# Performance work log

Measured on AMD Instinct MI355X. Metric: run time of the kernel, lower is better.

Reference implementation:

```python
import jax, jax.numpy as jnp
import numpy as np

N_NODES = 100000


def _sage_conv(x, edge_index, W_l, b_l, W_r):
    # PyG SAGEConv (aggr='mean', root_weight=True, normalize=False):
    # out = lin_l(mean_{j in N(i)} x_j) + lin_r(x_i)
    src, dst = edge_index[0], edge_index[1]
    n = x.shape[0]
    agg = jax.ops.segment_sum(x[src], dst, num_segments=n)
    cnt = jax.ops.segment_sum(jnp.ones((src.shape[0],), x.dtype), dst, num_segments=n)
    agg = agg / jnp.maximum(cnt, 1.0)[:, None]
    return agg @ W_l + b_l + x @ W_r


def setup_inputs() -> dict:
    key = jax.random.key(0)
    ks = jax.random.split(key, 12)
    in_dim, hidden = 384, 128
    x = jax.random.normal(ks[0], (N_NODES, in_dim), dtype=jnp.float32)
    edge_index = jax.random.randint(ks[1], (2, 3200000), 0, N_NODES, dtype=jnp.int32)
    pos_edge_label_index = jax.random.randint(ks[2], (2, 500000), 0, N_NODES, dtype=jnp.int32)
    neg_edge_label_index = jax.random.randint(ks[3], (2, 500000), 0, N_NODES, dtype=jnp.int32)
    s1 = 1.0 / np.sqrt(in_dim)
    s2 = 1.0 / np.sqrt(hidden)
    return {
        "x": x,
        "edge_index": edge_index,
        "pos_edge_label_index": pos_edge_label_index,
        "neg_edge_label_index": neg_edge_label_index,
        "W_l1": jax.random.uniform(ks[4], (in_dim, hidden), jnp.float32, -s1, s1),
        "b_l1": jnp.zeros((hidden,), jnp.float32),
        "W_r1": jax.random.uniform(ks[5], (in_dim, hidden), jnp.float32, -s1, s1),
        "W_l2": jax.random.uniform(ks[6], (hidden, hidden), jnp.float32, -s2, s2),
        "b_l2": jnp.zeros((hidden,), jnp.float32),
        "W_r2": jax.random.uniform(ks[7], (hidden, hidden), jnp.float32, -s2, s2),
        "W_lin": jax.random.uniform(ks[8], (2 * hidden, 1), jnp.float32, -s2, s2),
        "b_lin": jnp.zeros((1,), jnp.float32),
    }


def reference(x, edge_index, pos_edge_label_index, neg_edge_label_index,
              W_l1, b_l1, W_r1, W_l2, b_l2, W_r2, W_lin, b_lin):
    h = _sage_conv(x, edge_index, W_l1, b_l1, W_r1)
    h = jax.nn.relu(h)
    h = _sage_conv(h, edge_index, W_l2, b_l2, W_r2)

    def score(idx):
        pair = jnp.concatenate([h[idx[0]], h[idx[1]]], axis=1)  # [E, 2*hidden]
        return (pair @ W_lin + b_lin).reshape(-1)

    return score(pos_edge_label_index), score(neg_edge_label_index)
```

## Files before the change

kernel.cpp:

```cpp
#include <hip/hip_runtime.h>

#define IN_DIM 384
#define HID    128
#define NPB    256
#define BCAP   16384
#define LCAP   10240

#define AS1 __attribute__((address_space(1)))
#define AS3 __attribute__((address_space(3)))

typedef _Float16 half8 __attribute__((ext_vector_type(8)));
typedef _Float16 half2t __attribute__((ext_vector_type(2)));
typedef __fp16 fp16x2 __attribute__((ext_vector_type(2)));
typedef float floatx4 __attribute__((ext_vector_type(4)));
typedef float floatx2 __attribute__((ext_vector_type(2)));

__global__ void zero_i32(int* __restrict__ p, int n) {
  int i = blockIdx.x * 256 + threadIdx.x;
  if (i < n) p[i] = 0;
}

__global__ __launch_bounds__(512) void partition_kernel(
    const int* __restrict__ src, const int* __restrict__ dst, int E, int nB,
    int* __restrict__ bCur, unsigned* __restrict__ bucketData) {
  __shared__ int hist[391];
  __shared__ int gbase[391];
  const int t = threadIdx.x;
  const int b0 = blockIdx.x * 8192;

  for (int i = t; i < nB; i += 512) hist[i] = 0;
  __syncthreads();
#pragma unroll
  for (int i = 0; i < 16; ++i) {
    int e = b0 + i * 512 + t;
    if (e < E) atomicAdd(&hist[dst[e] >> 8], 1);
  }
  __syncthreads();
  for (int i = t; i < nB; i += 512) {
    int h = hist[i];
    gbase[i] = h ? (i * BCAP + atomicAdd(&bCur[i], h)) : 0;
    hist[i] = 0;
  }
  __syncthreads();
#pragma unroll
  for (int i = 0; i < 16; ++i) {
    int e = b0 + i * 512 + t;
    if (e < E) {
      int d = dst[e];
      int b = d >> 8;
      int r = atomicAdd(&hist[b], 1);
      bucketData[gbase[b] + r] = ((unsigned)(d & 255) << 17) | (unsigned)src[e];
    }
  }
}

__global__ __launch_bounds__(1024) void node_sort3(
    const unsigned* __restrict__ bucketData, const int* __restrict__ bCur,
    int N, int* __restrict__ sorted_src, int* __restrict__ rs, int* __restrict__ re) {
  extern __shared__ unsigned sdata[];
  __shared__ int hist[NPB];
  __shared__ int s[NPB];
  __shared__ int cur[NPB];
  const int b = blockIdx.x;
  const int t = threadIdx.x;
  const int start = b * BCAP;
  const int fill = bCur[b];
  if (t < NPB) hist[t] = 0;
  __syncthreads();
  for (int i = t; i < fill; i += 1024) {
    unsigned d = bucketData[start + i];
    if (i < LCAP) sdata[i] = d;
    atomicAdd(&hist[d >> 17], 1);
  }
  __syncthreads();
  int v = 0;
  if (t < NPB) { v = hist[t]; s[t] = v; }
  __syncthreads();
  for (int off = 1; off < NPB; off <<= 1) {
    int y = (t < NPB && t >= off) ? s[t - off] : 0;
    __syncthreads();
    if (t < NPB) s[t] += y;
    __syncthreads();
  }
  if (t < NPB) {
    int excl = s[t] - v;
    const int node = b * NPB + t;
    if (node < N) {
      rs[node] = start + excl;
      re[node] = start + excl + v;
    }
    cur[t] = start + excl;
  }
  __syncthreads();
  for (int i = t; i < fill; i += 1024) {
    unsigned d = (i < LCAP) ? sdata[i] : bucketData[start + i];
    int p = atomicAdd(&cur[d >> 17], 1);
    sorted_src[p] = (int)(d & 0x1FFFF);
  }
}

__global__ void pack_w2(const float* __restrict__ Wl, const float* __restrict__ Wr,
                        _Float16* __restrict__ Bp) {
  const float* __restrict__ W = blockIdx.z ? Wr : Wl;
  const int tn = blockIdx.x;
  const int ks = blockIdx.y;
  const int KS = gridDim.y;
  const int lane = threadIdx.x;
  const int n = tn * 16 + (lane & 15);
  const int kb = ks * 32 + (lane >> 4) * 8;
  half8 v;
#pragma unroll
  for (int j = 0; j < 8; ++j) v[j] = (_Float16)W[(size_t)(kb + j) * HID + n];
  *(half8*)(Bp + (((size_t)(blockIdx.z * 8 + tn) * KS + ks) * 64 + lane) * 8) = v;
}

__global__ __launch_bounds__(128) void pack_uv(
    const float* __restrict__ Wl2, const float* __restrict__ Wr2,
    const float* __restrict__ bl2, const float* __restrict__ Wlin,
    float* __restrict__ uv) {
  const int i = threadIdx.x;
  float ua = 0.f, ub = 0.f, va = 0.f, vb = 0.f;
  for (int o = 0; o < 128; ++o) {
    float wa = Wlin[o], wb = Wlin[128 + o];
    float l = Wl2[i * 128 + o], r = Wr2[i * 128 + o];
    ua += l * wa; ub += l * wb;
    va += r * wa; vb += r * wb;
  }
  uv[i] = ua; uv[128 + i] = ub; uv[256 + i] = va; uv[384 + i] = vb;
  if (i == 0) {
    float ca = 0.f, cb = 0.f;
    for (int o = 0; o < 128; ++o) {
      ca += bl2[o] * Wlin[o];
      cb += bl2[o] * Wlin[128 + o];
    }
    uv[512] = ca; uv[513] = cb;
  }
}

__device__ inline half2t cvt_pk(float a, float b) {
  fp16x2 r = __builtin_amdgcn_cvt_pkrtz(a, b);
  union { fp16x2 f; half2t h; } c;
  c.f = r;
  return c.h;
}

__global__ __launch_bounds__(512) void gemm_f32a(
    const float* __restrict__ A, int M,
    const _Float16* __restrict__ Bp,
    unsigned char* __restrict__ y8, _Float16* __restrict__ z1) {
  __shared__ float As[128 * 32];

  const int K = IN_DIM, KS = IN_DIM / 32;
  const int tid = threadIdx.x;
  const int lane = tid & 63;
  const int wid = tid >> 6;
  const int quad = lane >> 4;
  const int lm = lane & 15;
  const int row0 = (wid & 1) * 64;
  const int ct0 = (wid >> 1) * 4;
  const int blockRow = blockIdx.x * 128;

  const int srow = lane >> 3;
  const int scol = ((lane & 7) ^ (srow & 7)) * 4;
  const int grow0 = min(blockRow + wid * 16 + srow, M - 1);
  const int grow1 = min(blockRow + wid * 16 + 8 + srow, M - 1);

  floatx4 acc[16];
#pragma unroll
  for (int i = 0; i < 16; ++i) {
    acc[i][0] = 0.f; acc[i][1] = 0.f; acc[i][2] = 0.f; acc[i][3] = 0.f;
  }

  for (int ks = 0; ks < KS; ++ks) {
    const int k0 = ks * 32;
    __syncthreads();
    __builtin_amdgcn_global_load_lds(
        (const AS1 void*)(A + (size_t)grow0 * K + k0 + scol),
        (AS3 void*)(As + (wid * 16) * 32), 16, 0, 0);
    __builtin_amdgcn_global_load_lds(
        (const AS1 void*)(A + (size_t)grow1 * K + k0 + scol),
        (AS3 void*)(As + (wid * 16 + 8) * 32), 16, 0, 0);

    half8 bf[4];
#pragma unroll
    for (int ct = 0; ct < 4; ++ct)
      bf[ct] = *(const half8*)(Bp + (((size_t)(ct0 + ct) * KS + ks) * 64 + lane) * 8);

    __syncthreads();

    half8 af[4];
#pragma unroll
    for (int rt = 0; rt < 4; ++rt) {
      const int row = row0 + rt * 16 + lm;
      const int sw = row & 7;
      const floatx4 fA = *(const floatx4*)&As[(row * 8 + ((quad * 2) ^ sw)) * 4];
      const floatx4 fB = *(const floatx4*)&As[(row * 8 + ((quad * 2 + 1) ^ sw)) * 4];
      half2t h01 = cvt_pk(fA[0], fA[1]);
      half2t h23 = cvt_pk(fA[2], fA[3]);
      half2t h45 = cvt_pk(fB[0], fB[1]);
      half2t h67 = cvt_pk(fB[2], fB[3]);
      half8 a;
      a[0] = h01[0]; a[1] = h01[1]; a[2] = h23[0]; a[3] = h23[1];
      a[4] = h45[0]; a[5] = h45[1]; a[6] = h67[0]; a[7] = h67[1];
      af[rt] = a;
    }
#pragma unroll
    for (int rt = 0; rt < 4; ++rt)
#pragma unroll
      for (int ct = 0; ct < 4; ++ct)
        acc[rt * 4 + ct] =
            __builtin_amdgcn_mfma_f32_16x16x32_f16(af[rt], bf[ct], acc[rt * 4 + ct], 0, 0, 0);
  }

#pragma unroll
  for (int rt = 0; rt < 4; ++rt) {
#pragma unroll
    for (int r = 0; r < 4; ++r) {
      const int gm = blockRow + row0 + rt * 16 + quad * 4 + r;
      if (gm < M) {
#pragma unroll
        for (int ct = 0; ct < 4; ++ct) {
          const int tn = ct0 + ct;
          const float v = acc[rt * 4 + ct][r];
          if (tn < 8) {
            int p = __builtin_amdgcn_cvt_pk_fp8_f32(v, v, 0, false);
            y8[(size_t)gm * 128 + tn * 16 + lm] = (unsigned char)(p & 0xFF);
          } else {
            z1[(size_t)gm * 128 + (tn - 8) * 16 + lm] = (_Float16)v;
          }
        }
      }
    }
  }
}

__device__ inline float2 upk(unsigned u) {
  union { unsigned v; _Float16 h[2]; } c; c.v = u;
  return make_float2((float)c.h[0], (float)c.h[1]);
}

struct f32acc8 { floatx2 a, b, c, d; };
__device__ inline void f8acc(f32acc8& A, uint2 v) {
  A.a += __builtin_amdgcn_cvt_pk_f32_fp8(v.x, false);
  A.b += __builtin_amdgcn_cvt_pk_f32_fp8(v.x, true);
  A.c += __builtin_amdgcn_cvt_pk_f32_fp8(v.y, false);
  A.d += __builtin_amdgcn_cvt_pk_f32_fp8(v.y, true);
}
__device__ inline void f8merge(f32acc8& A, const f32acc8& B) {
  A.a += B.a; A.b += B.b; A.c += B.c; A.d += B.d;
}

__device__ inline f32acc8 gather_rows8(const unsigned char* __restrict__ y8,
                                       const int* __restrict__ sorted_src,
                                       int start, int end, int cl, int slot) {
  f32acc8 A0; A0.a = 0.f; A0.b = 0.f; A0.c = 0.f; A0.d = 0.f;
  f32acc8 A1 = A0;
  int k = start + slot;
  for (; k + 12 < end; k += 16) {
    int s0 = sorted_src[k];
    int s1 = sorted_src[k + 4];
    int s2 = sorted_src[k + 8];
    int s3 = sorted_src[k + 12];
    uint2 v0 = *(const uint2*)(y8 + (size_t)s0 * 128 + cl * 8);
    uint2 v1 = *(const uint2*)(y8 + (size_t)s1 * 128 + cl * 8);
    uint2 v2 = *(const uint2*)(y8 + (size_t)s2 * 128 + cl * 8);
    uint2 v3 = *(const uint2*)(y8 + (size_t)s3 * 128 + cl * 8);
    f8acc(A0, v0);
    f8acc(A1, v1);
    f8acc(A0, v2);
    f8acc(A1, v3);
  }
  if (k + 4 < end) {
    int s0 = sorted_src[k];
    int s1 = sorted_src[k + 4];
    uint2 v0 = *(const uint2*)(y8 + (size_t)s0 * 128 + cl * 8);
    uint2 v1 = *(const uint2*)(y8 + (size_t)s1 * 128 + cl * 8);
    f8acc(A0, v0);
    f8acc(A1, v1);
    k += 8;
  }
  if (k < end) {
    uint2 v = *(const uint2*)(y8 + (size_t)sorted_src[k] * 128 + cl * 8);
    f8acc(A0, v);
  }
  f8merge(A0, A1);
#pragma unroll
  for (int off = 16; off < 64; off <<= 1) {
    f32acc8 o;
    o.a[0] = __shfl_xor(A0.a[0], off, 64); o.a[1] = __shfl_xor(A0.a[1], off, 64);
    o.b[0] = __shfl_xor(A0.b[0], off, 64); o.b[1] = __shfl_xor(A0.b[1], off, 64);
    o.c[0] = __shfl_xor(A0.c[0], off, 64); o.c[1] = __shfl_xor(A0.c[1], off, 64);
    o.d[0] = __shfl_xor(A0.d[0], off, 64); o.d[1] = __shfl_xor(A0.d[1], off, 64);
    f8merge(A0, o);
  }
  return A0;
}

__global__ __launch_bounds__(256) void agg_relu8_dot(
    const unsigned char* __restrict__ y8, const unsigned* __restrict__ z1u,
    const int* __restrict__ sorted_src,
    const int* __restrict__ rs, const int* __restrict__ re,
    const float* __restrict__ bias, const float* __restrict__ uv,
    float2* __restrict__ t, float2* __restrict__ r, int N) {
  const int w = threadIdx.x >> 6;
  const int lane = threadIdx.x & 63;
  const int cl = lane & 15;
  const int slot = lane >> 4;
  const int node = blockIdx.x * 4 + w;
  if (node >= N) return;
  const int start = rs[node];
  const int end = re[node];
  f32acc8 A = gather_rows8(y8, sorted_src, start, end, cl, slot);
  if (slot == 0) {
    const int deg = end - start;
    const float inv = 1.f / (float)max(deg, 1);
    uint4 z4 = *(const uint4*)(z1u + (size_t)node * 64 + cl * 4);
    const unsigned zv[4] = {z4.x, z4.y, z4.z, z4.w};
    const floatx2 av[4] = {A.a, A.b, A.c, A.d};
    float hv[8];
#pragma unroll
    for (int q = 0; q < 4; ++q) {
      const int c = cl * 8 + q * 2;
      float2 z = upk(zv[q]);
      hv[2 * q]     = fmaxf(av[q][0] * inv + bias[c] + z.x, 0.f);
      hv[2 * q + 1] = fmaxf(av[q][1] * inv + bias[c + 1] + z.y, 0.f);
    }
    float ta = 0.f, tb = 0.f, ra = 0.f, rb = 0.f;
#pragma unroll
    for (int j = 0; j < 8; ++j) {
      const int c = cl * 8 + j;
      ta += hv[j] * uv[c];
      tb += hv[j] * uv[128 + c];
      ra += hv[j] * uv[256 + c];
      rb += hv[j] * uv[384 + c];
    }
#pragma unroll
    for (int off = 1; off < 16; off <<= 1) {
      ta += __shfl_xor(ta, off, 64);
      tb += __shfl_xor(tb, off, 64);
      ra += __shfl_xor(ra, off, 64);
      rb += __shfl_xor(rb, off, 64);
    }
    if (cl == 0) {
      t[node] = make_float2(ta, tb);
      r[node] = make_float2(ra + uv[512], rb + uv[513]);
    }
  }
}

__global__ __launch_bounds__(256) void agg_t(
    const float2* __restrict__ t, const int* __restrict__ sorted_src,
    const int* __restrict__ rs, const int* __restrict__ re,
    const float2* __restrict__ r,
    float* __restrict__ sa, float* __restrict__ sb, int N) {
  const int w = threadIdx.x >> 6;
  const int lane = threadIdx.x & 63;
  const int es = lane & 15;
  const int ns = lane >> 4;
  const int node = blockIdx.x * 16 + w * 4 + ns;
  if (node >= N) return;
  const int start = rs[node];
  const int end = re[node];
  float a = 0.f, b = 0.f;
  for (int k = start + es; k < end; k += 16) {
    float2 v = t[sorted_src[k]];
    a += v.x;
    b += v.y;
  }
#pragma unroll
  for (int off = 1; off < 16; off <<= 1) {
    a += __shfl_xor(a, off, 64);
    b += __shfl_xor(b, off, 64);
  }
  if (es == 0) {
    const int deg = end - start;
    const float inv = 1.f / (float)max(deg, 1);
    float2 rr = r[node];
    sa[node] = a * inv + rr.x;
    sb[node] = b * inv + rr.y;
  }
}

__global__ void score2(const int* __restrict__ pos, const int* __restrict__ neg,
                       int Ep, int En,
                       const float* __restrict__ sa, const float* __restrict__ sb,
                       const float* __restrict__ blin, float* __restrict__ out) {
  int e = blockIdx.x * 256 + threadIdx.x;
  if (e < Ep) {
    out[e] = sa[pos[e]] + sb[pos[Ep + e]] + blin[0];
  } else if (e < Ep + En) {
    int i = e - Ep;
    out[Ep + i] = sa[neg[i]] + sb[neg[En + i]] + blin[0];
  }
}

extern "C" void kernel_launch(void* const* d_in, const int* in_sizes, int n_in,
                              void* d_out, int out_size, void* d_ws, size_t ws_size,
                              hipStream_t stream) {
  (void)n_in; (void)out_size; (void)ws_size;
  const float* x    = (const float*)d_in[0];
  const int*   ei   = (const int*)d_in[1];
  const int*   pos  = (const int*)d_in[2];
  const int*   neg  = (const int*)d_in[3];
  const float* Wl1  = (const float*)d_in[4];
  const float* bl1  = (const float*)d_in[5];
  const float* Wr1  = (const float*)d_in[6];
  const float* Wl2  = (const float*)d_in[7];
  const float* bl2  = (const float*)d_in[8];
  const float* Wr2  = (const float*)d_in[9];
  const float* Wlin = (const float*)d_in[10];
  const float* blin = (const float*)d_in[11];

  const int N  = in_sizes[0] / IN_DIM;
  const int E  = in_sizes[1] / 2;
  const int Ep = in_sizes[2] / 2;
  const int En = in_sizes[3] / 2;
  const int* e_src = ei;
  const int* e_dst = ei + E;

  char* ws = (char*)d_ws;
  size_t off = 0;
  auto carve = [&](size_t bytes) -> char* {
    char* p = ws + off;
    off += (bytes + 255) & ~(size_t)255;
    return p;
  };
  const int nB = (N + NPB - 1) / NPB;
  const int KS1 = IN_DIM / 32;

  int*           rs     = (int*)carve((size_t)N * 4);
  int*           re     = (int*)carve((size_t)N * 4);
  int*           bCur   = (int*)carve(512 * 4);
  unsigned*      bData  = (unsigned*)carve((size_t)nB * BCAP * 4);
  int*           sorted = (int*)carve((size_t)nB * BCAP * 4);
  float*         sa     = (float*)carve((size_t)N * 4);
  float*         sb     = (float*)carve((size_t)N * 4);
  _Float16*      Bp1    = (_Float16*)carve((size_t)16 * KS1 * 64 * 8 * 2);
  float*         uv     = (float*)carve(516 * 4);
  float2*        tbuf   = (float2*)carve((size_t)N * 8);
  float2*        rbuf   = (float2*)carve((size_t)N * 8);
  unsigned char* y8     = (unsigned char*)carve((size_t)N * 128);
  _Float16*      z1     = (_Float16*)carve((size_t)N * 128 * 2);

  const int gemmBlocks = (N + 127) / 128;
  const int partBlocks = (E + 8191) / 8192;

  hipLaunchKernelGGL(zero_i32, dim3(2), dim3(256), 0, stream, bCur, 512);
  hipLaunchKernelGGL(partition_kernel, dim3(partBlocks), dim3(512), 0, stream,
                     e_src, e_dst, E, nB, bCur, bData);
  hipLaunchKernelGGL(node_sort3, dim3(nB), dim3(1024), LCAP * 4, stream,
                     bData, bCur, N, sorted, rs, re);

  hipLaunchKernelGGL(pack_w2, dim3(8, KS1, 2), dim3(64), 0, stream, Wl1, Wr1, Bp1);
  hipLaunchKernelGGL(pack_uv, dim3(1), dim3(128), 0, stream, Wl2, Wr2, bl2, Wlin, uv);

  hipLaunchKernelGGL(gemm_f32a, dim3(gemmBlocks), dim3(512), 0, stream,
                     x, N, Bp1, y8, z1);
  hipLaunchKernelGGL(agg_relu8_dot, dim3((N + 3) / 4), dim3(256), 0, stream,
                     y8, (const unsigned*)z1, sorted, rs, re, bl1, uv, tbuf, rbuf, N);
  hipLaunchKernelGGL(agg_t, dim3((N + 15) / 16), dim3(256), 0, stream,
                     tbuf, sorted, rs, re, rbuf, sa, sb, N);

  float* out = (float*)d_out;
  hipLaunchKernelGGL(score2, dim3((Ep + En + 255) / 256), dim3(256), 0, stream,
                     pos, neg, Ep, En, sa, sb, blin, out);
}
```

Measured before the change: 476.1 us.

## Process nodes in descending-degree order in aggregation kernels for load balance

```diff
diff --git a/kernel.cpp b/kernel.cpp
--- a/kernel.cpp
+++ b/kernel.cpp
@@ -56,7 +56,8 @@
 
 __global__ __launch_bounds__(1024) void node_sort3(
     const unsigned* __restrict__ bucketData, const int* __restrict__ bCur,
-    int N, int* __restrict__ sorted_src, int* __restrict__ rs, int* __restrict__ re) {
+    int N, int* __restrict__ sorted_src, int* __restrict__ rs, int* __restrict__ re,
+    int* __restrict__ dhist) {
   extern __shared__ unsigned sdata[];
   __shared__ int hist[NPB];
   __shared__ int s[NPB];
@@ -88,6 +89,7 @@
     if (node < N) {
       rs[node] = start + excl;
       re[node] = start + excl + v;
+      atomicAdd(&dhist[255 - min(v, 255)], 1);
     }
     cur[t] = start + excl;
   }
@@ -96,6 +98,33 @@
     unsigned d = (i < LCAP) ? sdata[i] : bucketData[start + i];
     int p = atomicAdd(&cur[d >> 17], 1);
     sorted_src[p] = (int)(d & 0x1FFFF);
+  }
+}
+
+__global__ __launch_bounds__(256) void scan_bins(
+    const int* __restrict__ dhist, int* __restrict__ dcur) {
+  __shared__ int s[256];
+  const int t = threadIdx.x;
+  int v = dhist[t];
+  s[t] = v;
+  __syncthreads();
+  for (int off = 1; off < 256; off <<= 1) {
+    int y = (t >= off) ? s[t - off] : 0;
+    __syncthreads();
+    s[t] += y;
+    __syncthreads();
+  }
+  dcur[t] = s[t] - v;
+}
+
+__global__ __launch_bounds__(256) void scatter_order(
+    const int* __restrict__ rs, const int* __restrict__ re, int N,
+    int* __restrict__ dcur, int* __restrict__ order) {
+  const int node = blockIdx.x * 256 + threadIdx.x;
+  if (node < N) {
+    int key = 255 - min(re[node] - rs[node], 255);
+    int p = atomicAdd(&dcur[key], 1);
+    order[p] = node;
   }
 }
 
@@ -298,7 +327,7 @@
 
 __global__ __launch_bounds__(256) void agg_relu8_dot(
     const unsigned char* __restrict__ y8, const unsigned* __restrict__ z1u,
-    const int* __restrict__ sorted_src,
+    const int* __restrict__ sorted_src, const int* __restrict__ order,
     const int* __restrict__ rs, const int* __restrict__ re,
     const float* __restrict__ bias, const float* __restrict__ uv,
     float2* __restrict__ t, float2* __restrict__ r, int N) {
@@ -306,8 +335,9 @@
   const int lane = threadIdx.x & 63;
   const int cl = lane & 15;
   const int slot = lane >> 4;
-  const int node = blockIdx.x * 4 + w;
-  if (node >= N) return;
+  const int idx = blockIdx.x * 4 + w;
+  if (idx >= N) return;
+  const int node = order[idx];
   const int start = rs[node];
   const int end = re[node];
   f32acc8 A = gather_rows8(y8, sorted_src, start, end, cl, slot);
@@ -350,6 +380,7 @@
 
 __global__ __launch_bounds__(256) void agg_t(
     const float2* __restrict__ t, const int* __restrict__ sorted_src,
+    const int* __restrict__ order,
     const int* __restrict__ rs, const int* __restrict__ re,
     const float2* __restrict__ r,
     float* __restrict__ sa, float* __restrict__ sb, int N) {
@@ -357,8 +388,9 @@
   const int lane = threadIdx.x & 63;
   const int es = lane & 15;
   const int ns = lane >> 4;
-  const int node = blockIdx.x * 16 + w * 4 + ns;
-  if (node >= N) return;
+  const int idx = blockIdx.x * 16 + w * 4 + ns;
+  if (idx >= N) return;
+  const int node = order[idx];
   const int start = rs[node];
   const int end = re[node];
   float a = 0.f, b = 0.f;
@@ -431,6 +463,9 @@
   int*           rs     = (int*)carve((size_t)N * 4);
   int*           re     = (int*)carve((size_t)N * 4);
   int*           bCur   = (int*)carve(512 * 4);
+  int*           dhist  = (int*)carve(256 * 4);
+  int*           dcur   = (int*)carve(256 * 4);
+  int*           order  = (int*)carve((size_t)N * 4);
   unsigned*      bData  = (unsigned*)carve((size_t)nB * BCAP * 4);
   int*           sorted = (int*)carve((size_t)nB * BCAP * 4);
   float*         sa     = (float*)carve((size_t)N * 4);
@@ -445,11 +480,14 @@
   const int gemmBlocks = (N + 127) / 128;
   const int partBlocks = (E + 8191) / 8192;
 
-  hipLaunchKernelGGL(zero_i32, dim3(2), dim3(256), 0, stream, bCur, 512);
+  hipLaunchKernelGGL(zero_i32, dim3(3), dim3(256), 0, stream, bCur, 512 + 256);
   hipLaunchKernelGGL(partition_kernel, dim3(partBlocks), dim3(512), 0, stream,
                      e_src, e_dst, E, nB, bCur, bData);
   hipLaunchKernelGGL(node_sort3, dim3(nB), dim3(1024), LCAP * 4, stream,
-                     bData, bCur, N, sorted, rs, re);
+                     bData, bCur, N, sorted, rs, re, dhist);
+  hipLaunchKernelGGL(scan_bins, dim3(1), dim3(256), 0, stream, dhist, dcur);
+  hipLaunchKernelGGL(scatter_order, dim3((N + 255) / 256), dim3(256), 0, stream,
+                     rs, re, N, dcur, order);
 
   hipLaunchKernelGGL(pack_w2, dim3(8, KS1, 2), dim3(64), 0, stream, Wl1, Wr1, Bp1);
   hipLaunchKernelGGL(pack_uv, dim3(1), dim3(128), 0, stream, Wl2, Wr2, bl2, Wlin, uv);
@@ -457,9 +495,10 @@
   hipLaunchKernelGGL(gemm_f32a, dim3(gemmBlocks), dim3(512), 0, stream,
                      x, N, Bp1, y8, z1);
   hipLaunchKernelGGL(agg_relu8_dot, dim3((N + 3) / 4), dim3(256), 0, stream,
-                     y8, (const unsigned*)z1, sorted, rs, re, bl1, uv, tbuf, rbuf, N);
+                     y8, (const unsigned*)z1, sorted, order, rs, re, bl1, uv,
+                     tbuf, rbuf, N);
   hipLaunchKernelGGL(agg_t, dim3((N + 15) / 16), dim3(256), 0, stream,
-                     tbuf, sorted, rs, re, rbuf, sa, sb, N);
+                     tbuf, sorted, order, rs, re, rbuf, sa, sb, N);
 
   float* out = (float*)d_out;
   hipLaunchKernelGGL(score2, dim3((Ep + En + 255) / 256), dim3(256), 0, stream,
```

After: 833.2 us. 1.75x slower.
